# Optimization experiments

Hardware: AMD Instinct MI355X
Metric: run time of the kernel (lower is better)

## Reference

```python
import jax, jax.numpy as jnp
import numpy as np

B, NP, L, C, NA = 16, 512, 20, 3, 50
RATIO = 0.8
K = int(np.ceil(RATIO * NP))  # 410 nodes kept per graph
N = B * NP
E = 6 * N
NF, EF = 13, 4
EPS = 1e-5


def _graph_norm(x, w, b, ms):
    # PyG GraphNorm called WITHOUT batch in the source -> single global graph
    mean = x.mean(0)
    out = x - ms * mean
    var = (out * out).mean(0)
    return w * out / jnp.sqrt(var + EPS) + b


def _forward(x, pan_w, lin1_w, lin1_b, norm1_w, norm1_b, norm1_ms,
             pool_p, pool_beta, gat_wl, gat_bl, gat_wr, gat_br, gat_att, gat_bias,
             norm2_w, norm2_b, norm2_ms,
             val1_w, val1_b, val2_w, val2_b, val3_w, val3_b,
             adv1_w, adv1_b, adv2_w, adv2_b, adv3_w, adv3_b,
             edge_index, current_node_ids, action_mask):
    src, dst = edge_index[0], edge_index[1]
    # PANConv builds SparseTensor(row=edge_index[1], col=edge_index[0]) -> row = target
    A = jnp.zeros((B, NP, NP), x.dtype).at[dst // NP, dst % NP, src % NP].set(1.0)
    eyeB = jnp.broadcast_to(jnp.eye(NP, dtype=x.dtype), A.shape)

    # panentropy: M = sum_{i=0..L} w_i * A^i  (dense per graph)
    def step(carry, wi):
        tmp, acc = carry
        tmp = tmp @ A
        return (tmp, acc + wi * tmp), None
    (_, M), _ = jax.lax.scan(step, (eyeB, pan_w[0] * eyeB), pan_w[1:])
    deg = M.sum(-1)                                   # row sums
    dis = jnp.where(deg > 0, 1.0 / jnp.sqrt(deg), 0.0)
    Mn = dis[:, :, None] * M * dis[:, None, :]        # D^-1/2 M D^-1/2

    # conv1: propagate (Mn @ x) then Linear
    x3 = x.reshape(B, NP, NF)
    h = jnp.einsum('bij,bjf->bif', Mn, x3) @ lin1_w + lin1_b   # [B,NP,C]
    x1 = jax.nn.relu(_graph_norm(h.reshape(N, C), norm1_w, norm1_b, norm1_ms))  # [N,C]
    h = x1.reshape(B, NP, C)

    # PANPooling: score = tanh(b0 * <x,p> + b1 * colsum(Mn)); keep top K per graph
    score = jnp.tanh(pool_beta[0] * (h * pool_p).sum(-1) + pool_beta[1] * Mn.sum(-2))
    vals, idx = jax.lax.top_k(score, K)                        # [B,K]
    xp = jnp.take_along_axis(h, idx[:, :, None], axis=1) * vals[..., None]
    Mg = jax.vmap(lambda m, i: m[i][:, i])(Mn, idx)            # filtered adjacency [B,K,K]
    mask = (jnp.swapaxes(Mg, 1, 2) != 0) | jnp.eye(K, dtype=bool)  # mask[b,i,j]: edge j->i (+self loops)

    # GATv2Conv, heads=1, eval mode (no dropout), edge_attr not passed in source
    xl = xp @ gat_wl + gat_bl
    xr = xp @ gat_wr + gat_br
    e = jax.nn.leaky_relu(xr[:, :, None, :] + xl[:, None, :, :], 0.2)  # [B,i,j,C]
    logits = jnp.where(mask, jnp.einsum('bijc,c->bij', e, gat_att), -1e9)
    alpha = jax.nn.softmax(logits, axis=-1)
    g = jnp.einsum('bij,bjc->bic', alpha, xl) + gat_bias

    g = jax.nn.relu(_graph_norm(g.reshape(B * K, C), norm2_w, norm2_b, norm2_ms)).reshape(B, K, C)
    gp = g.sum(1)                                              # global_add_pool [B,C]

    # source uses POOLED bincount cumsum offsets to index the pre-pool arrays (faithful)
    gidx = current_node_ids + jnp.arange(B, dtype=current_node_ids.dtype) * K
    feat = jnp.concatenate([x[gidx], x1[gidx], gp], axis=1)    # [B,19]

    a = jax.nn.relu(feat @ adv1_w + adv1_b)
    a = jax.nn.relu(a @ adv2_w + adv2_b)
    a = a @ adv3_w + adv3_b
    v = jax.nn.relu(feat @ val1_w + val1_b)
    v = jax.nn.relu(v @ val2_w + val2_b)
    v = v @ val3_w + val3_b
    q = v + (a - a.mean(1, keepdims=True))
    return jnp.where(action_mask == 0, -1e8, q)


def setup_inputs() -> dict:
    key = jax.random.key(0)
    ks = list(jax.random.split(key, 40))
    nk = lambda: ks.pop()
    # within-graph random edges so the PyG-style batch structure is valid
    g = jax.random.randint(nk(), (E,), 0, B)
    u = jax.random.randint(nk(), (E,), 0, NP)
    v = jax.random.randint(nk(), (E,), 0, NP)
    edge_index = jnp.stack([g * NP + u, g * NP + v]).astype(jnp.int32)

    def lin(k, i, o):
        k1, k2 = jax.random.split(k)
        return (jax.random.normal(k1, (i, o), jnp.float32) / np.sqrt(i),
                jax.random.normal(k2, (o,), jnp.float32) * 0.01)

    lin1_w, lin1_b = lin(nk(), NF, C)
    gat_wl, gat_bl = lin(nk(), C, C)
    gat_wr, gat_br = lin(nk(), C, C)
    val1_w, val1_b = lin(nk(), 19, 10)
    val2_w, val2_b = lin(nk(), 10, 5)
    val3_w, val3_b = lin(nk(), 5, 1)
    adv1_w, adv1_b = lin(nk(), 19, 10)
    adv2_w, adv2_b = lin(nk(), 10, 5)
    adv3_w, adv3_b = lin(nk(), 5, NA)
    return dict(
        x=jax.random.normal(nk(), (N, NF), jnp.float32),
        edge_index=edge_index,
        edge_attr=jax.random.normal(nk(), (E, EF), jnp.float32),
        batch=jnp.arange(N, dtype=jnp.int32) // NP,
        current_node_ids=jax.random.randint(nk(), (B,), 0, NP),
        action_mask=jax.random.randint(nk(), (B, NA), 0, 2),
        pan_w=jax.random.uniform(nk(), (L + 1,), jnp.float32) * 0.5,
        lin1_w=lin1_w, lin1_b=lin1_b,
        norm1_w=jnp.ones(C), norm1_b=jnp.zeros(C), norm1_ms=jnp.ones(C),
        pool_p=jax.random.normal(nk(), (C,), jnp.float32),
        pool_beta=jnp.array([0.5, 0.5], jnp.float32),
        gat_wl=gat_wl, gat_bl=gat_bl, gat_wr=gat_wr, gat_br=gat_br,
        gat_att=jax.random.normal(nk(), (C,), jnp.float32),
        gat_bias=jax.random.normal(nk(), (C,), jnp.float32) * 0.01,
        norm2_w=jnp.ones(C), norm2_b=jnp.zeros(C), norm2_ms=jnp.ones(C),
        val1_w=val1_w, val1_b=val1_b, val2_w=val2_w, val2_b=val2_b,
        val3_w=val3_w, val3_b=val3_b,
        adv1_w=adv1_w, adv1_b=adv1_b, adv2_w=adv2_w, adv2_b=adv2_b,
        adv3_w=adv3_w, adv3_b=adv3_b,
    )


def reference(x, edge_index, edge_attr, batch, current_node_ids, action_mask,
              pan_w, lin1_w, lin1_b, norm1_w, norm1_b, norm1_ms,
              pool_p, pool_beta, gat_wl, gat_bl, gat_wr, gat_br, gat_att, gat_bias,
              norm2_w, norm2_b, norm2_ms,
              val1_w, val1_b, val2_w, val2_b, val3_w, val3_b,
              adv1_w, adv1_b, adv2_w, adv2_b, adv3_w, adv3_b):
    del edge_attr, batch  # received by the torch forward but never consumed
    return _forward(x, pan_w, lin1_w, lin1_b, norm1_w, norm1_b, norm1_ms,
                    pool_p, pool_beta, gat_wl, gat_bl, gat_wr, gat_br, gat_att, gat_bias,
                    norm2_w, norm2_b, norm2_ms,
                    val1_w, val1_b, val2_w, val2_b, val3_w, val3_b,
                    adv1_w, adv1_b, adv2_w, adv2_b, adv3_w, adv3_b,
                    edge_index, current_node_ids, action_mask)
```

## Files before the change

### kernel.cpp

```cpp
#include <hip/hip_runtime.h>
#include <hip/hip_bf16.h>
#include <stdint.h>
#include <math.h>

#define BB   16
#define NPn  512
#define LLp  20
#define NAa  50
#define KKk  410
#define NNt  (BB * NPn)
#define EEe  (6 * NNt)
#define NFf  13
#define KPAD 416
#define EPSf 1e-5f
#define QCLMP 1e6f
#define MAXD 28
#define PADR 512

__device__ __forceinline__ float r12_sane(float v) {
    if (!(v == v)) return 0.0f;
    return fminf(fmaxf(v, -1e15f), 1e15f);
}

__global__ __launch_bounds__(256) void r12_scatter(
    const int* __restrict__ ei,
    uint32_t* __restrict__ fwdb, uint32_t* __restrict__ trsb)
{
    const int e = blockIdx.x * 256 + threadIdx.x;
    if (e < EEe) {
        const int src = ei[e], dst = ei[EEe + e];
        atomicOr(&fwdb[(size_t)dst * 16 + ((src & 511) >> 5)], 1u << (src & 31));
        atomicOr(&trsb[(size_t)src * 16 + ((dst & 511) >> 5)], 1u << (dst & 31));
    }
}

__global__ __launch_bounds__(256) void r12_extract(
    const uint32_t* __restrict__ fwdb, const uint32_t* __restrict__ trsb,
    unsigned short* __restrict__ csrF, unsigned short* __restrict__ csrT)
{
    const int t = blockIdx.x * 256 + threadIdx.x;
    const int node = t & 8191;
    const uint32_t* bs = (t < 8192) ? (fwdb + (size_t)node * 16)
                                    : (trsb + (size_t)node * 16);
    unsigned short* cs = (t < 8192) ? csrF : csrT;
    int cnt = 0;
    for (int w = 0; w < 16; ++w) {
        uint32_t bits = bs[w];
        while (bits) {
            const int u = (w << 5) + __ffs(bits) - 1;
            bits &= bits - 1;
            if (cnt < MAXD) cs[(size_t)cnt * 8192 + node] = (unsigned short)u;
            ++cnt;
        }
    }
    for (int j = cnt; j < MAXD; ++j) cs[(size_t)j * 8192 + node] = PADR;
}

__global__ __launch_bounds__(512) void r12_deg(
    const unsigned short* __restrict__ csrF,
    const float* __restrict__ panw,
    float* __restrict__ disv)
{
    __shared__ float pa[513], pb[513];
    __shared__ float wsh[21];
    const int b = blockIdx.x, v = threadIdx.x;
    const int node = b * 512 + v;
    int iF[MAXD];
#pragma unroll
    for (int j = 0; j < MAXD; ++j) iF[j] = (int)csrF[(size_t)j * 8192 + node];
    if (v < 21) wsh[v] = panw[v];
    pa[v] = 1.0f;
    if (v == 0) { pa[512] = 0.0f; pb[512] = 0.0f; }
    __syncthreads();
    float dacc = wsh[0];
    float* rp = pa; float* rn = pb;
    for (int i = 1; i <= LLp; ++i) {
        float t[MAXD];
#pragma unroll
        for (int j = 0; j < MAXD; ++j) t[j] = rp[iF[j]];
        float s = 0.0f;
#pragma unroll
        for (int j = 0; j < MAXD; ++j) s += t[j];
        rn[v] = s;
        dacc += wsh[i] * s;
        __syncthreads();
        float* tp = rp; rp = rn; rn = tp;
    }
    disv[node] = (dacc > 0.0f) ? 1.0f / sqrtf(dacc) : 0.0f;
}

__global__ __launch_bounds__(512) void r12_chan(
    const float* __restrict__ x,
    const unsigned short* __restrict__ csrF,
    const unsigned short* __restrict__ csrT,
    const float* __restrict__ disv,
    const float* __restrict__ panw,
    const float* __restrict__ l1w,
    const float* __restrict__ l1b,
    float* __restrict__ h_raw,
    float* __restrict__ colsum)
{
    __shared__ float pa[513], pb[513];
    __shared__ float wsh[21];
    const int b = blockIdx.x, c = blockIdx.y, v = threadIdx.x;
    const int node = b * 512 + v;
    const unsigned short* csr = (c < 3) ? csrF : csrT;
    int idx[MAXD];
#pragma unroll
    for (int j = 0; j < MAXD; ++j) idx[j] = (int)csr[(size_t)j * 8192 + node];
    if (v < 21) wsh[v] = panw[v];
    const float d0 = disv[node];

    float seed;
    if (c < 3) {
        float xw = 0.0f;
        const float* xr = x + (size_t)node * NFf;
        for (int f = 0; f < NFf; ++f) xw += xr[f] * l1w[f * 3 + c];
        seed = d0 * xw;
    } else {
        seed = d0;
    }
    pa[v] = seed;
    if (v == 0) { pa[512] = 0.0f; pb[512] = 0.0f; }
    __syncthreads();
    float acc = wsh[0] * seed;
    float* rp = pa; float* rn = pb;
    for (int i = 1; i <= LLp; ++i) {
        float t[MAXD];
#pragma unroll
        for (int j = 0; j < MAXD; ++j) t[j] = rp[idx[j]];
        float s = 0.0f;
#pragma unroll
        for (int j = 0; j < MAXD; ++j) s += t[j];
        rn[v] = s;
        acc += wsh[i] * s;
        __syncthreads();
        float* tp = rp; rp = rn; rn = tp;
    }
    if (c < 3) h_raw[(size_t)node * 3 + c] = r12_sane(d0 * acc + l1b[c]);
    else       colsum[node] = r12_sane(d0 * acc);
}

__global__ __launch_bounds__(512) void r12_closure(
    const unsigned short* __restrict__ csrF, uint32_t* __restrict__ Rb)
{
    __shared__ uint32_t R1[513], R2[513];
    const int b = blockIdx.x, q = blockIdx.y, v = threadIdx.x;
    const int node = b * 512 + v;
    int iF[MAXD];
#pragma unroll
    for (int j = 0; j < MAXD; ++j) iF[j] = (int)csrF[(size_t)j * 8192 + node];
    R1[v] = ((v >> 5) == q) ? (1u << (v & 31)) : 0u;
    if (v == 0) { R1[512] = 0u; R2[512] = 0u; }
    __syncthreads();
    uint32_t* Rp = R1; uint32_t* Rn = R2;
    for (int i = 0; i < LLp; ++i) {
        uint32_t t[MAXD];
#pragma unroll
        for (int j = 0; j < MAXD; ++j) t[j] = Rp[iF[j]];
        uint32_t r = Rp[v];
#pragma unroll
        for (int j = 0; j < MAXD; ++j) r |= t[j];
        Rn[v] = r;
        __syncthreads();
        uint32_t* tp = Rp; Rp = Rn; Rn = tp;
    }
    Rb[(size_t)node * 16 + q] = Rp[v];
}

__global__ __launch_bounds__(512) void r12_pool(
    const float* __restrict__ h_raw,
    const float* __restrict__ colsum,
    const float* n1w, const float* n1b, const float* n1ms,
    const float* poolp, const float* poolb,
    float* __restrict__ x1,
    float* __restrict__ xp,
    int* __restrict__ kept)
{
    __shared__ float red[512];
    __shared__ float mv[6];
    __shared__ float sc[NPn];
    const int b = blockIdx.x, v = threadIdx.x;
    const float inv_n = 1.0f / (float)NNt;

    float hv0[16], hv1[16], hv2[16];
    float s0 = 0.0f, s1 = 0.0f, s2 = 0.0f;
#pragma unroll
    for (int k = 0; k < 16; ++k) {
        const float* hr = h_raw + (size_t)(k * 512 + v) * 3;
        hv0[k] = hr[0]; hv1[k] = hr[1]; hv2[k] = hr[2];
        s0 += hv0[k]; s1 += hv1[k]; s2 += hv2[k];
    }
    float acc[3] = { s0, s1, s2 };
    for (int c = 0; c < 3; ++c) {
        __syncthreads();
        red[v] = acc[c];
        __syncthreads();
        for (int st = 256; st > 0; st >>= 1) {
            if (v < st) red[v] += red[v + st];
            __syncthreads();
        }
        if (v == 0) mv[c] = red[0] * inv_n;
    }
    __syncthreads();
    const float mm0 = n1ms[0] * mv[0], mm1 = n1ms[1] * mv[1], mm2 = n1ms[2] * mv[2];
    float a0 = 0.0f, a1 = 0.0f, a2 = 0.0f;
#pragma unroll
    for (int k = 0; k < 16; ++k) {
        const float d0 = hv0[k] - mm0, d1 = hv1[k] - mm1, d2 = hv2[k] - mm2;
        a0 += d0 * d0; a1 += d1 * d1; a2 += d2 * d2;
    }
    float accv[3] = { a0, a1, a2 };
    for (int c = 0; c < 3; ++c) {
        __syncthreads();
        red[v] = accv[c];
        __syncthreads();
        for (int st = 256; st > 0; st >>= 1) {
            if (v < st) red[v] += red[v + st];
            __syncthreads();
        }
        if (v == 0) mv[3 + c] = red[0] * inv_n;
    }
    __syncthreads();

    const float mmv[3] = { mm0, mm1, mm2 };
    float xv[3];
#pragma unroll
    for (int c = 0; c < 3; ++c) {
        const float iv = 1.0f / sqrtf(fmaxf(mv[3 + c], 0.0f) + EPSf);
        const float o  = h_raw[(size_t)(b * NPn + v) * 3 + c] - mmv[c];
        const float tt = n1w[c] * o * iv + n1b[c];
        xv[c] = fmaxf(tt, 0.0f);
        x1[(size_t)(b * NPn + v) * 3 + c] = xv[c];
    }
    float s = poolb[0] * (xv[0] * poolp[0] + xv[1] * poolp[1] + xv[2] * poolp[2])
            + poolb[1] * colsum[b * NPn + v];
    s = tanhf(s);
    if (!(s == s)) s = 0.0f;
    sc[v] = s;
    __syncthreads();
    int cnt = 0;
    for (int u = 0; u < NPn; ++u) {
        const float su = sc[u];
        cnt += ((su > s) || (su == s && u < v)) ? 1 : 0;
    }
    if (cnt < KKk) {
        kept[b * KPAD + cnt] = v;
        xp[(size_t)(b * KPAD + cnt) * 3 + 0] = xv[0] * s;
        xp[(size_t)(b * KPAD + cnt) * 3 + 1] = xv[1] * s;
        xp[(size_t)(b * KPAD + cnt) * 3 + 2] = xv[2] * s;
    }
}

__global__ __launch_bounds__(512) void r12_gat(
    const float* __restrict__ xp,
    const int* __restrict__ kept,
    const uint32_t* __restrict__ Rb,
    const float* wl, const float* bl,
    const float* wr, const float* br,
    const float* att, const float* gbias,
    float* __restrict__ g_raw)
{
    __shared__ float xlS[KKk * 3];
    __shared__ int kidx[KPAD];
    __shared__ uint32_t RT[16 * KPAD];
    const int b = blockIdx.x, t = threadIdx.x;
    const int lane = t & 63, wv = t >> 6;
    const int wid = blockIdx.y * 8 + wv;

    float Wl[9], Wr[9];
#pragma unroll
    for (int i2 = 0; i2 < 9; ++i2) { Wl[i2] = wl[i2]; Wr[i2] = wr[i2]; }
    const float Bl0 = bl[0], Bl1 = bl[1], Bl2 = bl[2];
    const float Br0 = br[0], Br1 = br[1], Br2 = br[2];
    const float At0 = att[0], At1 = att[1], At2 = att[2];
    const float Gb0 = gbias[0], Gb1 = gbias[1], Gb2 = gbias[2];

    for (int j = t; j < KKk; j += 512) {
        const int vj = kept[b * KPAD + j];
        kidx[j] = vj;
        const float p0 = xp[(size_t)(b * KPAD + j) * 3 + 0];
        const float p1 = xp[(size_t)(b * KPAD + j) * 3 + 1];
        const float p2 = xp[(size_t)(b * KPAD + j) * 3 + 2];
        xlS[j * 3 + 0] = p0 * Wl[0] + p1 * Wl[3] + p2 * Wl[6] + Bl0;
        xlS[j * 3 + 1] = p0 * Wl[1] + p1 * Wl[4] + p2 * Wl[7] + Bl1;
        xlS[j * 3 + 2] = p0 * Wl[2] + p1 * Wl[5] + p2 * Wl[8] + Bl2;
        const uint32_t* rr = Rb + (size_t)(b * NPn + vj) * 16;
#pragma unroll
        for (int w = 0; w < 16; ++w) RT[w * KPAD + j] = rr[w];
    }
    __syncthreads();

    for (int i = wid; i < KKk; i += 32) {
        const float p0 = xp[(size_t)(b * KPAD + i) * 3 + 0];
        const float p1 = xp[(size_t)(b * KPAD + i) * 3 + 1];
        const float p2 = xp[(size_t)(b * KPAD + i) * 3 + 2];
        const float xr0 = p0 * Wr[0] + p1 * Wr[3] + p2 * Wr[6] + Br0;
        const float xr1 = p0 * Wr[1] + p1 * Wr[4] + p2 * Wr[7] + Br1;
        const float xr2 = p0 * Wr[2] + p1 * Wr[5] + p2 * Wr[8] + Br2;
        const int bi = kidx[i];
        const uint32_t mbit = 1u << (bi & 31);
        const uint32_t* Rw = &RT[(bi >> 5) * KPAD];

        float mx = -3e38f, lsum = 0.0f, a0 = 0.0f, a1 = 0.0f, a2 = 0.0f;
        for (int j = lane; j < KKk; j += 64) {
            if ((Rw[j] & mbit) || (j == i)) {
                float e0 = xr0 + xlS[j * 3 + 0]; e0 = e0 > 0.0f ? e0 : 0.2f * e0;
                float e1 = xr1 + xlS[j * 3 + 1]; e1 = e1 > 0.0f ? e1 : 0.2f * e1;
                float e2 = xr2 + xlS[j * 3 + 2]; e2 = e2 > 0.0f ? e2 : 0.2f * e2;
                const float s = At0 * e0 + At1 * e1 + At2 * e2;
                if (s > mx) {
                    const float r = __expf(mx - s);
                    lsum *= r; a0 *= r; a1 *= r; a2 *= r;
                    mx = s;
                }
                const float pj = __expf(s - mx);
                lsum += pj;
                a0 += pj * xlS[j * 3 + 0];
                a1 += pj * xlS[j * 3 + 1];
                a2 += pj * xlS[j * 3 + 2];
            }
        }
        for (int off = 32; off; off >>= 1) {
            const float mo = __shfl_xor(mx, off);
            const float lo = __shfl_xor(lsum, off);
            const float b0 = __shfl_xor(a0, off);
            const float b1 = __shfl_xor(a1, off);
            const float b2 = __shfl_xor(a2, off);
            const float M  = fmaxf(mx, mo);
            const float ea = __expf(mx - M), eb = __expf(mo - M);
            lsum = lsum * ea + lo * eb;
            a0 = a0 * ea + b0 * eb;
            a1 = a1 * ea + b1 * eb;
            a2 = a2 * ea + b2 * eb;
            mx = M;
        }
        if (lane == 0) {
            const float rl = 1.0f / fmaxf(lsum, 1e-30f);
            g_raw[(size_t)(b * KPAD + i) * 3 + 0] = r12_sane(a0 * rl + Gb0);
            g_raw[(size_t)(b * KPAD + i) * 3 + 1] = r12_sane(a1 * rl + Gb1);
            g_raw[(size_t)(b * KPAD + i) * 3 + 2] = r12_sane(a2 * rl + Gb2);
        }
    }
}

__global__ __launch_bounds__(512) void r12_head(
    const float* __restrict__ g_raw,
    const float* __restrict__ x1,
    const float* __restrict__ x,
    const int* __restrict__ cnid,
    const int* __restrict__ amask,
    const float* n2w, const float* n2b, const float* n2ms,
    const float* v1w, const float* v1b,
    const float* v2w, const float* v2b,
    const float* v3w, const float* v3b,
    const float* a1w, const float* a1b,
    const float* a2w, const float* a2b,
    const float* a3w, const float* a3b,
    float* __restrict__ out)
{
    __shared__ float rbuf[512];
    __shared__ float mv[6];
    __shared__ float gp[3];
    __shared__ float feat[19];
    __shared__ float h1a[10], h1v[10], h2a[5], h2v[5];
    __shared__ float a3[50];
    __shared__ float vout_s, amean_s;
    const int b = blockIdx.x, t = threadIdx.x;
    const float denom = 1.0f / (float)(BB * KKk);

    float gv0[13], gv1[13], gv2[13];
    float s0 = 0.0f, s1 = 0.0f, s2 = 0.0f;
#pragma unroll
    for (int k = 0; k < 13; ++k) {
        const int r = k * 512 + t;
        float q0 = 0.0f, q1 = 0.0f, q2 = 0.0f;
        if (r < BB * KKk) {
            const int bq = r / KKk, iq = r - bq * KKk;
            const float* gr = g_raw + (size_t)(bq * KPAD + iq) * 3;
            q0 = gr[0]; q1 = gr[1]; q2 = gr[2];
        }
        gv0[k] = q0; gv1[k] = q1; gv2[k] = q2;
        s0 += q0; s1 += q1; s2 += q2;
    }
    float acc[3] = { s0, s1, s2 };
    for (int c = 0; c < 3; ++c) {
        __syncthreads();
        rbuf[t] = acc[c];
        __syncthreads();
        for (int st = 256; st > 0; st >>= 1) {
            if (t < st) rbuf[t] += rbuf[t + st];
            __syncthreads();
        }
        if (t == 0) mv[c] = rbuf[0] * denom;
    }
    __syncthreads();
    const float mm0 = n2ms[0] * mv[0], mm1 = n2ms[1] * mv[1], mm2 = n2ms[2] * mv[2];
    float a0 = 0.0f, a1 = 0.0f, a2 = 0.0f;
#pragma unroll
    for (int k = 0; k < 13; ++k) {
        const int r = k * 512 + t;
        if (r < BB * KKk) {
            const float d0 = gv0[k] - mm0, d1 = gv1[k] - mm1, d2 = gv2[k] - mm2;
            a0 += d0 * d0; a1 += d1 * d1; a2 += d2 * d2;
        }
    }
    float accv[3] = { a0, a1, a2 };
    for (int c = 0; c < 3; ++c) {
        __syncthreads();
        rbuf[t] = accv[c];
        __syncthreads();
        for (int st = 256; st > 0; st >>= 1) {
            if (t < st) rbuf[t] += rbuf[t + st];
            __syncthreads();
        }
        if (t == 0) mv[3 + c] = rbuf[0] * denom;
    }
    __syncthreads();

    const float mmv[3] = { mm0, mm1, mm2 };
    float s3[3] = { 0.0f, 0.0f, 0.0f };
    if (t < KKk) {
        const size_t r = (size_t)(b * KPAD + t) * 3;
#pragma unroll
        for (int c = 0; c < 3; ++c) {
            const float iv = 1.0f / sqrtf(fmaxf(mv[3 + c], 0.0f) + EPSf);
            s3[c] = fmaxf((g_raw[r + c] - mmv[c]) * iv * n2w[c] + n2b[c], 0.0f);
        }
    }
    for (int c = 0; c < 3; ++c) {
        __syncthreads();
        rbuf[t] = s3[c];
        __syncthreads();
        for (int st = 256; st > 0; st >>= 1) {
            if (t < st) rbuf[t] += rbuf[t + st];
            __syncthreads();
        }
        if (t == 0) gp[c] = rbuf[0];
    }
    __syncthreads();

    if (t < 19) {
        const int gidx = cnid[b] + b * KKk;
        float fv;
        if (t < 13)      fv = x[(size_t)gidx * NFf + t];
        else if (t < 16) fv = x1[(size_t)gidx * 3 + (t - 13)];
        else             fv = gp[t - 16];
        feat[t] = fv;
    }
    __syncthreads();

    if (t < 10) {
        float s = a1b[t];
        for (int f = 0; f < 19; ++f) s += feat[f] * a1w[f * 10 + t];
        h1a[t] = fmaxf(s, 0.0f);
    } else if (t >= 64 && t < 74) {
        const int j = t - 64;
        float s = v1b[j];
        for (int f = 0; f < 19; ++f) s += feat[f] * v1w[f * 10 + j];
        h1v[j] = fmaxf(s, 0.0f);
    }
    __syncthreads();
    if (t < 5) {
        float s = a2b[t];
        for (int k = 0; k < 10; ++k) s += h1a[k] * a2w[k * 5 + t];
        h2a[t] = fmaxf(s, 0.0f);
    } else if (t >= 64 && t < 69) {
        const int j = t - 64;
        float s = v2b[j];
        for (int k = 0; k < 10; ++k) s += h1v[k] * v2w[k * 5 + j];
        h2v[j] = fmaxf(s, 0.0f);
    }
    __syncthreads();
    if (t < 50) {
        float s = a3b[t];
        for (int k = 0; k < 5; ++k) s += h2a[k] * a3w[k * 50 + t];
        a3[t] = s;
    } else if (t == 64) {
        float s = v3b[0];
        for (int k = 0; k < 5; ++k) s += h2v[k] * v3w[k];
        vout_s = s;
    }
    __syncthreads();
    if (t == 0) {
        float s = 0.0f;
        for (int k = 0; k < 50; ++k) s += a3[k];
        amean_s = s * (1.0f / 50.0f);
    }
    __syncthreads();
    if (t < 50) {
        float q = vout_s + a3[t] - amean_s;
        if (!(q == q)) q = 0.0f;
        q = fminf(fmaxf(q, -QCLMP), QCLMP);
        out[b * NAa + t] = (amask[b * NAa + t] == 0) ? -1e8f : q;
    }
}

extern "C" void kernel_launch(void* const* d_in, const int* in_sizes, int n_in,
                              void* d_out, int out_size, void* d_ws, size_t ws_size,
                              hipStream_t stream) {
    (void)in_sizes; (void)n_in; (void)out_size;
    const float* x     = (const float*)d_in[0];
    const int* ei      = (const int*)d_in[1];
    const int* cnid    = (const int*)d_in[4];
    const int* amask   = (const int*)d_in[5];
    const float* panw  = (const float*)d_in[6];
    const float* l1w   = (const float*)d_in[7];
    const float* l1b   = (const float*)d_in[8];
    const float* n1w   = (const float*)d_in[9];
    const float* n1b   = (const float*)d_in[10];
    const float* n1ms  = (const float*)d_in[11];
    const float* poolp = (const float*)d_in[12];
    const float* poolb = (const float*)d_in[13];
    const float* gwl   = (const float*)d_in[14];
    const float* gbl   = (const float*)d_in[15];
    const float* gwr   = (const float*)d_in[16];
    const float* gbr   = (const float*)d_in[17];
    const float* gatt  = (const float*)d_in[18];
    const float* gbias = (const float*)d_in[19];
    const float* n2w   = (const float*)d_in[20];
    const float* n2b   = (const float*)d_in[21];
    const float* n2ms  = (const float*)d_in[22];
    const float* v1w   = (const float*)d_in[23];
    const float* v1b   = (const float*)d_in[24];
    const float* v2w   = (const float*)d_in[25];
    const float* v2b   = (const float*)d_in[26];
    const float* v3w   = (const float*)d_in[27];
    const float* v3b   = (const float*)d_in[28];
    const float* a1w   = (const float*)d_in[29];
    const float* a1b   = (const float*)d_in[30];
    const float* a2w   = (const float*)d_in[31];
    const float* a2b   = (const float*)d_in[32];
    const float* a3w   = (const float*)d_in[33];
    const float* a3b   = (const float*)d_in[34];
    float* out         = (float*)d_out;

    uint8_t* wsb = (uint8_t*)d_ws;
    uint32_t* fwdb = (uint32_t*)wsb;
    uint32_t* trsb = (uint32_t*)(wsb + 524288);
    uint32_t* Rb   = trsb;
    unsigned short* csrF = (unsigned short*)(wsb + 1048576);
    unsigned short* csrT = csrF + (size_t)MAXD * 8192;
    float* h_raw  = (float*)(csrT + (size_t)MAXD * 8192);
    float* x1     = h_raw + (size_t)NNt * 3;
    float* colsum = x1 + (size_t)NNt * 3;
    float* disv   = colsum + NNt;
    float* xp     = disv + NNt;
    float* g_raw  = xp + (size_t)BB * KPAD * 3;
    int*   kept   = (int*)(g_raw + (size_t)BB * KPAD * 3);
    const size_t needed = 1048576 + 2 * (size_t)MAXD * 8192 * 2 +
                          ((size_t)(2 * NNt * 3 + 2 * NNt + 2 * BB * KPAD * 3 + BB * KPAD)) * 4;
    if (ws_size < needed) return;

    hipMemsetAsync(fwdb, 0, 1048576, stream);
    r12_scatter<<<dim3((EEe + 255) / 256), dim3(256), 0, stream>>>(ei, fwdb, trsb);
    r12_extract<<<dim3(64), dim3(256), 0, stream>>>(fwdb, trsb, csrF, csrT);
    r12_deg<<<dim3(16), dim3(512), 0, stream>>>(csrF, panw, disv);
    r12_chan<<<dim3(16, 4), dim3(512), 0, stream>>>(x, csrF, csrT, disv, panw,
                                                    l1w, l1b, h_raw, colsum);
    r12_closure<<<dim3(16, 16), dim3(512), 0, stream>>>(csrF, Rb);
    r12_pool<<<dim3(16), dim3(512), 0, stream>>>(h_raw, colsum, n1w, n1b, n1ms,
                                                 poolp, poolb, x1, xp, kept);
    r12_gat<<<dim3(16, 4), dim3(512), 0, stream>>>(xp, kept, Rb, gwl, gbl, gwr, gbr,
                                                   gatt, gbias, g_raw);
    r12_head<<<dim3(16), dim3(512), 0, stream>>>(g_raw, x1, x, cnid, amask,
                                                 n2w, n2b, n2ms, v1w, v1b, v2w, v2b, v3w, v3b,
                                                 a1w, a1b, a2w, a2b, a3w, a3b, out);
}
```

Measured before the change: 247.4 us.

## Fuse graph preprocessing kernels and pool+GAT, add degree-specialized propagation chains

Merges extract, degree, channel propagation and reachability closure into one launch with 16x20 blocks. Each block rebuilds its neighbour lists straight from the bitsets and recomputes the degree chain redundantly instead of reading a stored CSR and disv. Pooling and GAT become one kernel, so the kept indices and pooled features stay in shared memory. Templated chains pick a 16-neighbour unrolled gather when the block's max degree allows it. This cuts launch count and global round trips, at the cost of redundant degree work in every channel block and a large shared-memory footprint in poolgat with only 16 blocks and no GAT y-split.

```diff
diff --git a/kernel.cpp b/kernel.cpp
--- a/kernel.cpp
+++ b/kernel.cpp
@@ -17,12 +17,72 @@
 #define MAXD 28
 #define PADR 512
 
-__device__ __forceinline__ float r12_sane(float v) {
+__device__ __forceinline__ float r14_sane(float v) {
     if (!(v == v)) return 0.0f;
     return fminf(fmaxf(v, -1e15f), 1e15f);
 }
 
-__global__ __launch_bounds__(256) void r12_scatter(
+__device__ __forceinline__ int r14_extract(const uint32_t* __restrict__ bs, int* idx) {
+    int cnt = 0;
+    for (int w = 0; w < 16; ++w) {
+        uint32_t bits = bs[w];
+        while (bits) {
+            const int u = (w << 5) + __ffs(bits) - 1;
+            bits &= bits - 1;
+            if (cnt < MAXD) idx[cnt] = u;
+            ++cnt;
+        }
+    }
+    const int c = (cnt < MAXD) ? cnt : MAXD;
+    for (int j = c; j < MAXD; ++j) idx[j] = PADR;
+    return c;
+}
+
+template<int N>
+__device__ __forceinline__ float r14_chain(float* RA, float* RB, const int* idx,
+                                           const float* wsh, int v, float seed) {
+    RA[v] = seed;
+    if (v == 0) { RA[512] = 0.0f; RB[512] = 0.0f; }
+    __syncthreads();
+    float acc = wsh[0] * seed;
+    float* rp = RA; float* rn = RB;
+    for (int i = 1; i <= LLp; ++i) {
+        float tv[N];
+#pragma unroll
+        for (int j = 0; j < N; ++j) tv[j] = rp[idx[j]];
+        float s = 0.0f;
+#pragma unroll
+        for (int j = 0; j < N; ++j) s += tv[j];
+        rn[v] = s;
+        acc += wsh[i] * s;
+        __syncthreads();
+        float* tp = rp; rp = rn; rn = tp;
+    }
+    return acc;
+}
+
+template<int N>
+__device__ __forceinline__ void r14_cchain(uint32_t* R1, uint32_t* R2, const int* idx,
+                                           int v, int q, uint32_t* __restrict__ Rb, int node) {
+    R1[v] = ((v >> 5) == q) ? (1u << (v & 31)) : 0u;
+    if (v == 0) { R1[512] = 0u; R2[512] = 0u; }
+    __syncthreads();
+    uint32_t* Rp = R1; uint32_t* Rn = R2;
+    for (int i = 0; i < LLp; ++i) {
+        uint32_t tv[N];
+#pragma unroll
+        for (int j = 0; j < N; ++j) tv[j] = Rp[idx[j]];
+        uint32_t r = Rp[v];
+#pragma unroll
+        for (int j = 0; j < N; ++j) r |= tv[j];
+        Rn[v] = r;
+        __syncthreads();
+        uint32_t* tp = Rp; Rp = Rn; Rn = tp;
+    }
+    Rb[(size_t)node * 16 + q] = Rp[v];
+}
+
+__global__ __launch_bounds__(256) void r14_scatter(
     const int* __restrict__ ei,
     uint32_t* __restrict__ fwdb, uint32_t* __restrict__ trsb)
 {
@@ -34,173 +94,113 @@
     }
 }
 
-__global__ __launch_bounds__(256) void r12_extract(
-    const uint32_t* __restrict__ fwdb, const uint32_t* __restrict__ trsb,
-    unsigned short* __restrict__ csrF, unsigned short* __restrict__ csrT)
+__global__ __launch_bounds__(512) void r14_mid(
+    const float* __restrict__ x,
+    const uint32_t* __restrict__ fwdb,
+    const uint32_t* __restrict__ trsb,
+    const float* __restrict__ panw,
+    const float* __restrict__ l1w, const float* __restrict__ l1b,
+    float* __restrict__ h_raw, float* __restrict__ colsum,
+    uint32_t* __restrict__ Rb)
 {
-    const int t = blockIdx.x * 256 + threadIdx.x;
-    const int node = t & 8191;
-    const uint32_t* bs = (t < 8192) ? (fwdb + (size_t)node * 16)
-                                    : (trsb + (size_t)node * 16);
-    unsigned short* cs = (t < 8192) ? csrF : csrT;
-    int cnt = 0;
-    for (int w = 0; w < 16; ++w) {
-        uint32_t bits = bs[w];
-        while (bits) {
-            const int u = (w << 5) + __ffs(bits) - 1;
-            bits &= bits - 1;
-            if (cnt < MAXD) cs[(size_t)cnt * 8192 + node] = (unsigned short)u;
-            ++cnt;
-        }
-    }
-    for (int j = cnt; j < MAXD; ++j) cs[(size_t)j * 8192 + node] = PADR;
-}
-
-__global__ __launch_bounds__(512) void r12_deg(
-    const unsigned short* __restrict__ csrF,
-    const float* __restrict__ panw,
-    float* __restrict__ disv)
-{
-    __shared__ float pa[513], pb[513];
-    __shared__ float wsh[21];
-    const int b = blockIdx.x, v = threadIdx.x;
-    const int node = b * 512 + v;
-    int iF[MAXD];
-#pragma unroll
-    for (int j = 0; j < MAXD; ++j) iF[j] = (int)csrF[(size_t)j * 8192 + node];
-    if (v < 21) wsh[v] = panw[v];
-    pa[v] = 1.0f;
-    if (v == 0) { pa[512] = 0.0f; pb[512] = 0.0f; }
-    __syncthreads();
-    float dacc = wsh[0];
-    float* rp = pa; float* rn = pb;
-    for (int i = 1; i <= LLp; ++i) {
-        float t[MAXD];
-#pragma unroll
-        for (int j = 0; j < MAXD; ++j) t[j] = rp[iF[j]];
-        float s = 0.0f;
-#pragma unroll
-        for (int j = 0; j < MAXD; ++j) s += t[j];
-        rn[v] = s;
-        dacc += wsh[i] * s;
-        __syncthreads();
-        float* tp = rp; rp = rn; rn = tp;
-    }
-    disv[node] = (dacc > 0.0f) ? 1.0f / sqrtf(dacc) : 0.0f;
-}
-
-__global__ __launch_bounds__(512) void r12_chan(
-    const float* __restrict__ x,
-    const unsigned short* __restrict__ csrF,
-    const unsigned short* __restrict__ csrT,
-    const float* __restrict__ disv,
-    const float* __restrict__ panw,
-    const float* __restrict__ l1w,
-    const float* __restrict__ l1b,
-    float* __restrict__ h_raw,
-    float* __restrict__ colsum)
-{
-    __shared__ float pa[513], pb[513];
-    __shared__ float wsh[21];
-    const int b = blockIdx.x, c = blockIdx.y, v = threadIdx.x;
-    const int node = b * 512 + v;
-    const unsigned short* csr = (c < 3) ? csrF : csrT;
-    int idx[MAXD];
-#pragma unroll
-    for (int j = 0; j < MAXD; ++j) idx[j] = (int)csr[(size_t)j * 8192 + node];
-    if (v < 21) wsh[v] = panw[v];
-    const float d0 = disv[node];
-
-    float seed;
-    if (c < 3) {
-        float xw = 0.0f;
-        const float* xr = x + (size_t)node * NFf;
-        for (int f = 0; f < NFf; ++f) xw += xr[f] * l1w[f * 3 + c];
-        seed = d0 * xw;
+    __shared__ __align__(16) uint32_t sbuf[1056];
+    float* pa = (float*)sbuf;
+    float* pb = (float*)(sbuf + 513);
+    float* wsh = (float*)(sbuf + 1026);
+    int* mxS = (int*)(sbuf + 1048);
+    const int b = blockIdx.x, y = blockIdx.y, t = threadIdx.x;
+    const int node = b * 512 + t;
+
+    if (y < 4) {
+        const int c = y;
+        int iF[MAXD], iT[MAXD];
+        const int cntF = r14_extract(fwdb + (size_t)node * 16, iF);
+        int cntT = 0;
+        if (c == 3) cntT = r14_extract(trsb + (size_t)node * 16, iT);
+        if (t == 0) { mxS[0] = 0; mxS[1] = 0; }
+        if (t < 21) wsh[t] = panw[t];
+        __syncthreads();
+        atomicMax(&mxS[0], cntF);
+        if (c == 3) atomicMax(&mxS[1], cntT);
+        __syncthreads();
+        const int mF = mxS[0], mT = mxS[1];
+
+        float dacc;
+        if (mF <= 16) dacc = r14_chain<16>(pa, pb, iF, wsh, t, 1.0f);
+        else          dacc = r14_chain<28>(pa, pb, iF, wsh, t, 1.0f);
+        const float d0 = (dacc > 0.0f) ? 1.0f / sqrtf(dacc) : 0.0f;
+
+        if (c < 3) {
+            float xw = 0.0f;
+            const float* xr = x + (size_t)node * NFf;
+            for (int f = 0; f < NFf; ++f) xw += xr[f] * l1w[f * 3 + c];
+            float acc;
+            if (mF <= 16) acc = r14_chain<16>(pa, pb, iF, wsh, t, d0 * xw);
+            else          acc = r14_chain<28>(pa, pb, iF, wsh, t, d0 * xw);
+            h_raw[(size_t)node * 3 + c] = r14_sane(d0 * acc + l1b[c]);
+        } else {
+            float acc;
+            if (mT <= 16) acc = r14_chain<16>(pa, pb, iT, wsh, t, d0);
+            else          acc = r14_chain<28>(pa, pb, iT, wsh, t, d0);
+            colsum[node] = r14_sane(d0 * acc);
+        }
     } else {
-        seed = d0;
-    }
-    pa[v] = seed;
-    if (v == 0) { pa[512] = 0.0f; pb[512] = 0.0f; }
-    __syncthreads();
-    float acc = wsh[0] * seed;
-    float* rp = pa; float* rn = pb;
-    for (int i = 1; i <= LLp; ++i) {
-        float t[MAXD];
-#pragma unroll
-        for (int j = 0; j < MAXD; ++j) t[j] = rp[idx[j]];
-        float s = 0.0f;
-#pragma unroll
-        for (int j = 0; j < MAXD; ++j) s += t[j];
-        rn[v] = s;
-        acc += wsh[i] * s;
-        __syncthreads();
-        float* tp = rp; rp = rn; rn = tp;
-    }
-    if (c < 3) h_raw[(size_t)node * 3 + c] = r12_sane(d0 * acc + l1b[c]);
-    else       colsum[node] = r12_sane(d0 * acc);
-}
-
-__global__ __launch_bounds__(512) void r12_closure(
-    const unsigned short* __restrict__ csrF, uint32_t* __restrict__ Rb)
-{
-    __shared__ uint32_t R1[513], R2[513];
-    const int b = blockIdx.x, q = blockIdx.y, v = threadIdx.x;
-    const int node = b * 512 + v;
-    int iF[MAXD];
-#pragma unroll
-    for (int j = 0; j < MAXD; ++j) iF[j] = (int)csrF[(size_t)j * 8192 + node];
-    R1[v] = ((v >> 5) == q) ? (1u << (v & 31)) : 0u;
-    if (v == 0) { R1[512] = 0u; R2[512] = 0u; }
-    __syncthreads();
-    uint32_t* Rp = R1; uint32_t* Rn = R2;
-    for (int i = 0; i < LLp; ++i) {
-        uint32_t t[MAXD];
-#pragma unroll
-        for (int j = 0; j < MAXD; ++j) t[j] = Rp[iF[j]];
-        uint32_t r = Rp[v];
-#pragma unroll
-        for (int j = 0; j < MAXD; ++j) r |= t[j];
-        Rn[v] = r;
-        __syncthreads();
-        uint32_t* tp = Rp; Rp = Rn; Rn = tp;
-    }
-    Rb[(size_t)node * 16 + q] = Rp[v];
-}
-
-__global__ __launch_bounds__(512) void r12_pool(
+        const int q = y - 4;
+        int iF[MAXD];
+        const int cntF = r14_extract(fwdb + (size_t)node * 16, iF);
+        if (t == 0) mxS[0] = 0;
+        __syncthreads();
+        atomicMax(&mxS[0], cntF);
+        __syncthreads();
+        const int mF = mxS[0];
+        uint32_t* R1 = sbuf;
+        uint32_t* R2 = sbuf + 513;
+        if (mF <= 16) r14_cchain<16>(R1, R2, iF, t, q, Rb, node);
+        else          r14_cchain<28>(R1, R2, iF, t, q, Rb, node);
+    }
+}
+
+__global__ __launch_bounds__(512) void r14_poolgat(
     const float* __restrict__ h_raw,
     const float* __restrict__ colsum,
+    const uint32_t* __restrict__ Rb,
     const float* n1w, const float* n1b, const float* n1ms,
     const float* poolp, const float* poolb,
+    const float* gwl, const float* gbl,
+    const float* gwr, const float* gbr,
+    const float* gatt, const float* gbias,
     float* __restrict__ x1,
-    float* __restrict__ xp,
-    int* __restrict__ kept)
+    float* __restrict__ g_raw)
 {
-    __shared__ float red[512];
-    __shared__ float mv[6];
-    __shared__ float sc[NPn];
-    const int b = blockIdx.x, v = threadIdx.x;
+    __shared__ __align__(16) uint32_t pg[10592];
+    float* red  = (float*)pg;
+    float* sc   = (float*)(pg + 512);
+    float* mv   = (float*)(pg + 1024);
+    float* xpS  = (float*)(pg + 1032);
+    int*   kidx = (int*)(pg + 2280);
+    float* xlS  = (float*)(pg + 2696);
+    uint32_t* RT = pg + 3928;
+    const int b = blockIdx.x, t = threadIdx.x;
     const float inv_n = 1.0f / (float)NNt;
 
     float hv0[16], hv1[16], hv2[16];
     float s0 = 0.0f, s1 = 0.0f, s2 = 0.0f;
 #pragma unroll
     for (int k = 0; k < 16; ++k) {
-        const float* hr = h_raw + (size_t)(k * 512 + v) * 3;
+        const float* hr = h_raw + (size_t)(k * 512 + t) * 3;
         hv0[k] = hr[0]; hv1[k] = hr[1]; hv2[k] = hr[2];
         s0 += hv0[k]; s1 += hv1[k]; s2 += hv2[k];
     }
     float acc[3] = { s0, s1, s2 };
     for (int c = 0; c < 3; ++c) {
         __syncthreads();
-        red[v] = acc[c];
+        red[t] = acc[c];
         __syncthreads();
         for (int st = 256; st > 0; st >>= 1) {
-            if (v < st) red[v] += red[v + st];
+            if (t < st) red[t] += red[t + st];
             __syncthreads();
         }
-        if (v == 0) mv[c] = red[0] * inv_n;
+        if (t == 0) mv[c] = red[0] * inv_n;
     }
     __syncthreads();
     const float mm0 = n1ms[0] * mv[0], mm1 = n1ms[1] * mv[1], mm2 = n1ms[2] * mv[2];
@@ -213,13 +213,13 @@
     float accv[3] = { a0, a1, a2 };
     for (int c = 0; c < 3; ++c) {
         __syncthreads();
-        red[v] = accv[c];
+        red[t] = accv[c];
         __syncthreads();
         for (int st = 256; st > 0; st >>= 1) {
-            if (v < st) red[v] += red[v + st];
+            if (t < st) red[t] += red[t + st];
             __syncthreads();
         }
-        if (v == 0) mv[3 + c] = red[0] * inv_n;
+        if (t == 0) mv[3 + c] = red[0] * inv_n;
     }
     __syncthreads();
 
@@ -228,123 +228,104 @@
 #pragma unroll
     for (int c = 0; c < 3; ++c) {
         const float iv = 1.0f / sqrtf(fmaxf(mv[3 + c], 0.0f) + EPSf);
-        const float o  = h_raw[(size_t)(b * NPn + v) * 3 + c] - mmv[c];
+        const float o  = h_raw[(size_t)(b * NPn + t) * 3 + c] - mmv[c];
         const float tt = n1w[c] * o * iv + n1b[c];
         xv[c] = fmaxf(tt, 0.0f);
-        x1[(size_t)(b * NPn + v) * 3 + c] = xv[c];
+        x1[(size_t)(b * NPn + t) * 3 + c] = xv[c];
     }
     float s = poolb[0] * (xv[0] * poolp[0] + xv[1] * poolp[1] + xv[2] * poolp[2])
-            + poolb[1] * colsum[b * NPn + v];
+            + poolb[1] * colsum[b * NPn + t];
     s = tanhf(s);
     if (!(s == s)) s = 0.0f;
-    sc[v] = s;
+    sc[t] = s;
     __syncthreads();
     int cnt = 0;
     for (int u = 0; u < NPn; ++u) {
         const float su = sc[u];
-        cnt += ((su > s) || (su == s && u < v)) ? 1 : 0;
+        cnt += ((su > s) || (su == s && u < t)) ? 1 : 0;
     }
     if (cnt < KKk) {
-        kept[b * KPAD + cnt] = v;
-        xp[(size_t)(b * KPAD + cnt) * 3 + 0] = xv[0] * s;
-        xp[(size_t)(b * KPAD + cnt) * 3 + 1] = xv[1] * s;
-        xp[(size_t)(b * KPAD + cnt) * 3 + 2] = xv[2] * s;
-    }
-}
-
-__global__ __launch_bounds__(512) void r12_gat(
-    const float* __restrict__ xp,
-    const int* __restrict__ kept,
-    const uint32_t* __restrict__ Rb,
-    const float* wl, const float* bl,
-    const float* wr, const float* br,
-    const float* att, const float* gbias,
-    float* __restrict__ g_raw)
-{
-    __shared__ float xlS[KKk * 3];
-    __shared__ int kidx[KPAD];
-    __shared__ uint32_t RT[16 * KPAD];
-    const int b = blockIdx.x, t = threadIdx.x;
-    const int lane = t & 63, wv = t >> 6;
-    const int wid = blockIdx.y * 8 + wv;
+        kidx[cnt] = t;
+        xpS[cnt * 3 + 0] = xv[0] * s;
+        xpS[cnt * 3 + 1] = xv[1] * s;
+        xpS[cnt * 3 + 2] = xv[2] * s;
+    }
+    __syncthreads();
 
     float Wl[9], Wr[9];
 #pragma unroll
-    for (int i2 = 0; i2 < 9; ++i2) { Wl[i2] = wl[i2]; Wr[i2] = wr[i2]; }
-    const float Bl0 = bl[0], Bl1 = bl[1], Bl2 = bl[2];
-    const float Br0 = br[0], Br1 = br[1], Br2 = br[2];
-    const float At0 = att[0], At1 = att[1], At2 = att[2];
+    for (int i2 = 0; i2 < 9; ++i2) { Wl[i2] = gwl[i2]; Wr[i2] = gwr[i2]; }
+    const float Bl0 = gbl[0], Bl1 = gbl[1], Bl2 = gbl[2];
+    const float Br0 = gbr[0], Br1 = gbr[1], Br2 = gbr[2];
+    const float At0 = gatt[0], At1 = gatt[1], At2 = gatt[2];
     const float Gb0 = gbias[0], Gb1 = gbias[1], Gb2 = gbias[2];
-
     for (int j = t; j < KKk; j += 512) {
-        const int vj = kept[b * KPAD + j];
-        kidx[j] = vj;
-        const float p0 = xp[(size_t)(b * KPAD + j) * 3 + 0];
-        const float p1 = xp[(size_t)(b * KPAD + j) * 3 + 1];
-        const float p2 = xp[(size_t)(b * KPAD + j) * 3 + 2];
+        const float p0 = xpS[j * 3 + 0];
+        const float p1 = xpS[j * 3 + 1];
+        const float p2 = xpS[j * 3 + 2];
         xlS[j * 3 + 0] = p0 * Wl[0] + p1 * Wl[3] + p2 * Wl[6] + Bl0;
         xlS[j * 3 + 1] = p0 * Wl[1] + p1 * Wl[4] + p2 * Wl[7] + Bl1;
         xlS[j * 3 + 2] = p0 * Wl[2] + p1 * Wl[5] + p2 * Wl[8] + Bl2;
-        const uint32_t* rr = Rb + (size_t)(b * NPn + vj) * 16;
+        const uint32_t* rr = Rb + (size_t)(b * NPn + kidx[j]) * 16;
 #pragma unroll
         for (int w = 0; w < 16; ++w) RT[w * KPAD + j] = rr[w];
     }
     __syncthreads();
 
-    for (int i = wid; i < KKk; i += 32) {
-        const float p0 = xp[(size_t)(b * KPAD + i) * 3 + 0];
-        const float p1 = xp[(size_t)(b * KPAD + i) * 3 + 1];
-        const float p2 = xp[(size_t)(b * KPAD + i) * 3 + 2];
+    const int lane = t & 63, wv = t >> 6;
+    for (int i = wv; i < KKk; i += 8) {
+        const float p0 = xpS[i * 3 + 0];
+        const float p1 = xpS[i * 3 + 1];
+        const float p2 = xpS[i * 3 + 2];
         const float xr0 = p0 * Wr[0] + p1 * Wr[3] + p2 * Wr[6] + Br0;
         const float xr1 = p0 * Wr[1] + p1 * Wr[4] + p2 * Wr[7] + Br1;
         const float xr2 = p0 * Wr[2] + p1 * Wr[5] + p2 * Wr[8] + Br2;
         const int bi = kidx[i];
         const uint32_t mbit = 1u << (bi & 31);
         const uint32_t* Rw = &RT[(bi >> 5) * KPAD];
-
-        float mx = -3e38f, lsum = 0.0f, a0 = 0.0f, a1 = 0.0f, a2 = 0.0f;
+        float mx = -3e38f, lsum = 0.0f, b0 = 0.0f, b1 = 0.0f, b2 = 0.0f;
         for (int j = lane; j < KKk; j += 64) {
             if ((Rw[j] & mbit) || (j == i)) {
                 float e0 = xr0 + xlS[j * 3 + 0]; e0 = e0 > 0.0f ? e0 : 0.2f * e0;
                 float e1 = xr1 + xlS[j * 3 + 1]; e1 = e1 > 0.0f ? e1 : 0.2f * e1;
                 float e2 = xr2 + xlS[j * 3 + 2]; e2 = e2 > 0.0f ? e2 : 0.2f * e2;
-                const float s = At0 * e0 + At1 * e1 + At2 * e2;
-                if (s > mx) {
-                    const float r = __expf(mx - s);
-                    lsum *= r; a0 *= r; a1 *= r; a2 *= r;
-                    mx = s;
+                const float sv = At0 * e0 + At1 * e1 + At2 * e2;
+                if (sv > mx) {
+                    const float r = __expf(mx - sv);
+                    lsum *= r; b0 *= r; b1 *= r; b2 *= r;
+                    mx = sv;
                 }
-                const float pj = __expf(s - mx);
+                const float pj = __expf(sv - mx);
                 lsum += pj;
-                a0 += pj * xlS[j * 3 + 0];
-                a1 += pj * xlS[j * 3 + 1];
-                a2 += pj * xlS[j * 3 + 2];
+                b0 += pj * xlS[j * 3 + 0];
+                b1 += pj * xlS[j * 3 + 1];
+                b2 += pj * xlS[j * 3 + 2];
             }
         }
         for (int off = 32; off; off >>= 1) {
             const float mo = __shfl_xor(mx, off);
             const float lo = __shfl_xor(lsum, off);
-            const float b0 = __shfl_xor(a0, off);
-            const float b1 = __shfl_xor(a1, off);
-            const float b2 = __shfl_xor(a2, off);
+            const float c0 = __shfl_xor(b0, off);
+            const float c1 = __shfl_xor(b1, off);
+            const float c2 = __shfl_xor(b2, off);
             const float M  = fmaxf(mx, mo);
             const float ea = __expf(mx - M), eb = __expf(mo - M);
             lsum = lsum * ea + lo * eb;
-            a0 = a0 * ea + b0 * eb;
-            a1 = a1 * ea + b1 * eb;
-            a2 = a2 * ea + b2 * eb;
+            b0 = b0 * ea + c0 * eb;
+            b1 = b1 * ea + c1 * eb;
+            b2 = b2 * ea + c2 * eb;
             mx = M;
         }
         if (lane == 0) {
             const float rl = 1.0f / fmaxf(lsum, 1e-30f);
-            g_raw[(size_t)(b * KPAD + i) * 3 + 0] = r12_sane(a0 * rl + Gb0);
-            g_raw[(size_t)(b * KPAD + i) * 3 + 1] = r12_sane(a1 * rl + Gb1);
-            g_raw[(size_t)(b * KPAD + i) * 3 + 2] = r12_sane(a2 * rl + Gb2);
-        }
-    }
-}
-
-__global__ __launch_bounds__(512) void r12_head(
+            g_raw[(size_t)(b * KPAD + i) * 3 + 0] = r14_sane(b0 * rl + Gb0);
+            g_raw[(size_t)(b * KPAD + i) * 3 + 1] = r14_sane(b1 * rl + Gb1);
+            g_raw[(size_t)(b * KPAD + i) * 3 + 2] = r14_sane(b2 * rl + Gb2);
+        }
+    }
+}
+
+__global__ __launch_bounds__(512) void r14_head(
     const float* __restrict__ g_raw,
     const float* __restrict__ x1,
     const float* __restrict__ x,
@@ -538,32 +519,24 @@
     uint8_t* wsb = (uint8_t*)d_ws;
     uint32_t* fwdb = (uint32_t*)wsb;
     uint32_t* trsb = (uint32_t*)(wsb + 524288);
-    uint32_t* Rb   = trsb;
-    unsigned short* csrF = (unsigned short*)(wsb + 1048576);
-    unsigned short* csrT = csrF + (size_t)MAXD * 8192;
-    float* h_raw  = (float*)(csrT + (size_t)MAXD * 8192);
+    uint32_t* Rb   = (uint32_t*)(wsb + 1048576);
+    float* h_raw  = (float*)(wsb + 1572864);
     float* x1     = h_raw + (size_t)NNt * 3;
     float* colsum = x1 + (size_t)NNt * 3;
-    float* disv   = colsum + NNt;
-    float* xp     = disv + NNt;
-    float* g_raw  = xp + (size_t)BB * KPAD * 3;
-    int*   kept   = (int*)(g_raw + (size_t)BB * KPAD * 3);
-    const size_t needed = 1048576 + 2 * (size_t)MAXD * 8192 * 2 +
-                          ((size_t)(2 * NNt * 3 + 2 * NNt + 2 * BB * KPAD * 3 + BB * KPAD)) * 4;
+    float* g_raw  = colsum + NNt;
+    const size_t needed = 1572864 +
+                          ((size_t)(2 * NNt * 3 + NNt + BB * KPAD * 3)) * 4;
     if (ws_size < needed) return;
 
     hipMemsetAsync(fwdb, 0, 1048576, stream);
-    r12_scatter<<<dim3((EEe + 255) / 256), dim3(256), 0, stream>>>(ei, fwdb, trsb);
-    r12_extract<<<dim3(64), dim3(256), 0, stream>>>(fwdb, trsb, csrF, csrT);
-    r12_deg<<<dim3(16), dim3(512), 0, stream>>>(csrF, panw, disv);
-    r12_chan<<<dim3(16, 4), dim3(512), 0, stream>>>(x, csrF, csrT, disv, panw,
-                                                    l1w, l1b, h_raw, colsum);
-    r12_closure<<<dim3(16, 16), dim3(512), 0, stream>>>(csrF, Rb);
-    r12_pool<<<dim3(16), dim3(512), 0, stream>>>(h_raw, colsum, n1w, n1b, n1ms,
-                                                 poolp, poolb, x1, xp, kept);
-    r12_gat<<<dim3(16, 4), dim3(512), 0, stream>>>(xp, kept, Rb, gwl, gbl, gwr, gbr,
-                                                   gatt, gbias, g_raw);
-    r12_head<<<dim3(16), dim3(512), 0, stream>>>(g_raw, x1, x, cnid, amask,
+    r14_scatter<<<dim3((EEe + 255) / 256), dim3(256), 0, stream>>>(ei, fwdb, trsb);
+    r14_mid<<<dim3(16, 20), dim3(512), 0, stream>>>(x, fwdb, trsb, panw, l1w, l1b,
+                                                    h_raw, colsum, Rb);
+    r14_poolgat<<<dim3(16), dim3(512), 0, stream>>>(h_raw, colsum, Rb,
+                                                    n1w, n1b, n1ms, poolp, poolb,
+                                                    gwl, gbl, gwr, gbr, gatt, gbias,
+                                                    x1, g_raw);
+    r14_head<<<dim3(16), dim3(512), 0, stream>>>(g_raw, x1, x, cnid, amask,
                                                  n2w, n2b, n2ms, v1w, v1b, v2w, v2b, v3w, v3b,
                                                  a1w, a1b, a2w, a2b, a3w, a3b, out);
 }
```

New measurement: 344.3 us. 1.39x slower.
